# Optimization experiments

Measured on AMD Instinct MI355X. Metric: run time of the kernel, lower is better.

Reference implementation:

```python
import jax, jax.numpy as jnp
import numpy as np
from jax.scipy.special import logsumexp

# Model config: alphabet='ACGTZY', collapse='ACGTCA' -> 4 canonical bases, 2 mods
NBASE = 4
NTRANS = 2 * NBASE * (NBASE + 1)          # 40 flip-flop transition states
CAN_NMODS = np.array([1, 1, 0, 0])        # mods per canonical base (A:Y, C:Z)
SIZE = NTRANS + 1 + int(CAN_NMODS.sum())  # 43 linear outputs
LARGE_LOG_VAL = np.float32(50000.0)
T, N, INSIZE = 2000, 128, 256


def _can_indices():
    """Per-canonical-base index groups into the mod block of the linear output."""
    idx, cur = [], 0
    for nm in CAN_NMODS:
        idx.append(np.concatenate([[0], np.arange(cur + 1, cur + 1 + nm)]))
        cur += nm
    return idx

CAN_INDICES = _can_indices()


def setup_inputs() -> dict:
    key = jax.random.key(0)
    k1, k2, k3 = jax.random.split(key, 3)
    x = jax.random.normal(k1, (T, N, INSIZE), dtype=jnp.float32)
    W = jax.random.normal(k2, (SIZE, INSIZE), dtype=jnp.float32) / np.float32(INSIZE ** 0.5)
    b = jax.random.normal(k3, (SIZE,), dtype=jnp.float32) * 0.1
    return {"x": x, "W": W, "b": b}


def global_norm_flipflop(scores):
    """Log-partition of the flip-flop CRF via a sequential log-space scan.

    scores: (T, N, 2*nbase*(nbase+1)).
    """
    Tn, Nn, _ = scores.shape
    # initial state: flip states uniform, flop states ~ -inf
    fwd0 = jnp.concatenate(
        [jnp.zeros((Nn, NBASE), scores.dtype),
         jnp.full((Nn, NBASE), -LARGE_LOG_VAL, scores.dtype)], axis=1)
    logZ0 = logsumexp(fwd0, axis=1, keepdims=True)
    fwd0 = fwd0 - logZ0

    def step(carry, scores_t):
        fwd, logZ = carry
        # (N, nbase+1, 2*nbase): dest-state x source-state transition scores
        curr = fwd[:, None, :] + scores_t.reshape(Nn, NBASE + 1, 2 * NBASE)
        base1 = logsumexp(curr[:, :NBASE], axis=2)                    # to-flip states
        base2 = jnp.logaddexp(curr[:, NBASE, :NBASE],
                              curr[:, NBASE, NBASE:])                 # to-flop (stay)
        new = jnp.concatenate([base1, base2], axis=1)                 # (N, 2*nbase)
        fac = logsumexp(new, axis=1, keepdims=True)
        return (new - fac, logZ + fac), None

    (_, logZ), _ = jax.lax.scan(step, (fwd0, logZ0), scores)
    return scores - logZ / np.float32(Tn)


def reference(x, W, b):
    # Linear projection: (T, N, insize) -> (T, N, size)
    y = jnp.einsum('tnf,cf->tnc', x, W) + b
    # Globally-normalized flip-flop transition scores
    trans = global_norm_flipflop(y[:, :, :NTRANS])
    # Per-canonical-base categorical (can + its mods) log-softmax scores
    mods = [jax.nn.log_softmax(y[:, :, NTRANS + idx], axis=2) for idx in CAN_INDICES]
    return jnp.concatenate([trans] + mods, axis=2)
```

## Files before the change

kernel.cpp:

```cpp
#include <hip/hip_runtime.h>

#define T_DIM 2000
#define N_DIM 128
#define IN_DIM 256
#define OUT_C 46
#define NROWS (T_DIM * N_DIM)
#define NCHUNK 250
#define CLEN 8
#define NSUPER 25
#define SLEN 10

typedef short bf16x8 __attribute__((ext_vector_type(8)));
typedef float f32x4 __attribute__((ext_vector_type(4)));

union F8U { bf16x8 v; uint32_t u[4]; };

__device__ __forceinline__ uint32_t cvtpk(float lo, float hi) {
  uint32_t r;
  asm("v_cvt_pk_bf16_f32 %0, %1, %2" : "=v"(r) : "v"(lo), "v"(hi));
  return r;
}

__device__ __forceinline__ float bf2f(unsigned short u) {
  uint32_t w = (uint32_t)u << 16;
  return __builtin_bit_cast(float, w);
}

#define LDSK 264
#define YPAD 132

__global__ __launch_bounds__(256, 3) void k1_gemm(const float* __restrict__ x,
                                                  const float* __restrict__ W,
                                                  const float* __restrict__ b,
                                                  unsigned short* __restrict__ wsYT,
                                                  float* __restrict__ wsMod) {
  __shared__ unsigned short Wl[43 * LDSK];
  __shared__ unsigned short Yst[2 * 40 * YPAD];
  const int tid  = threadIdx.x;
  const int lane = tid & 63;
  const int wv   = tid >> 6;
  const int ln   = lane & 15;
  const int lh   = lane >> 4;

  {
    uint32_t* Wd = reinterpret_cast<uint32_t*>(Wl);
#pragma unroll
    for (int it = 0; it < 22; ++it) {
      int e = tid + it * 256;
      if (e < 43 * 128) {
        int n = e >> 7, kp = e & 127;
        float2 w = *reinterpret_cast<const float2*>(W + (size_t)n * IN_DIM + 2 * kp);
        Wd[n * (LDSK / 2) + kp] = cvtpk(w.x, w.y);
      }
    }
  }
  float bias[3];
#pragma unroll
  for (int nt = 0; nt < 3; ++nt) {
    int n = nt * 16 + ln;
    bias[nt] = b[n > 42 ? 42 : n];
  }
  __syncthreads();

  const int rowbase = blockIdx.x * 256 + wv * 64;
  const float* xbase = x + (size_t)(rowbase + ln) * IN_DIM + lh * 8;

  f32x4 bufA[8], bufB[8];
  f32x4 zero = {0.f, 0.f, 0.f, 0.f};
  f32x4 acc[3] = {zero, zero, zero};

#define LOADH(BUF, T, HF) do {                                               \
    const float* _p = xbase + (size_t)(T) * (16 * IN_DIM) + (HF) * 128;      \
    _Pragma("unroll")                                                        \
    for (int _s = 0; _s < 4; ++_s) {                                         \
      BUF[_s]     = *reinterpret_cast<const f32x4*>(_p + _s * 32);           \
      BUF[_s + 4] = *reinterpret_cast<const f32x4*>(_p + _s * 32 + 4);       \
    }                                                                        \
  } while (0)

#define COMPH(BUF, HF) do {                                                  \
    _Pragma("unroll")                                                        \
    for (int _s2 = 0; _s2 < 4; ++_s2) {                                      \
      F8U _af;                                                               \
      _af.u[0] = cvtpk(BUF[_s2].x, BUF[_s2].y);                              \
      _af.u[1] = cvtpk(BUF[_s2].z, BUF[_s2].w);                              \
      _af.u[2] = cvtpk(BUF[_s2 + 4].x, BUF[_s2 + 4].y);                      \
      _af.u[3] = cvtpk(BUF[_s2 + 4].z, BUF[_s2 + 4].w);                      \
      const int _s = (HF) * 4 + _s2;                                         \
      _Pragma("unroll")                                                      \
      for (int _nt = 0; _nt < 3; ++_nt) {                                    \
        const bf16x8 _bf = *reinterpret_cast<const bf16x8*>(                 \
            &Wl[(_nt * 16 + ln) * LDSK + _s * 32 + lh * 8]);                 \
        acc[_nt] = __builtin_amdgcn_mfma_f32_16x16x32_bf16(_af.v, _bf,       \
                                                           acc[_nt], 0, 0, 0);\
      }                                                                      \
    }                                                                        \
  } while (0)

  LOADH(bufA, 0, 0);
  LOADH(bufB, 0, 1);
#pragma unroll 1
  for (int t = 0; t < 4; ++t) {
    COMPH(bufA, 0);
    if (t < 3) LOADH(bufA, t + 1, 0);
    COMPH(bufB, 1);
    if (t < 3) LOADH(bufB, t + 1, 1);
    const int R0   = rowbase + t * 16;
    const int tloc = (R0 >> 7) & 1;
    const int n0   = (R0 & 127) + lh * 4;
#pragma unroll
    for (int nt = 0; nt < 3; ++nt) {
      const int c = nt * 16 + ln;
      if (nt < 2 || ln < 8) {
        uint32_t d0 = cvtpk(acc[nt][0] + bias[nt], acc[nt][1] + bias[nt]);
        uint32_t d1 = cvtpk(acc[nt][2] + bias[nt], acc[nt][3] + bias[nt]);
        uint2 v; v.x = d0; v.y = d1;
        *reinterpret_cast<uint2*>(&Yst[(tloc * 40 + c) * YPAD + n0]) = v;
      } else if (ln < 11) {
        const int tt = R0 >> 7;
        float4 v;
        v.x = acc[2][0] + bias[2]; v.y = acc[2][1] + bias[2];
        v.z = acc[2][2] + bias[2]; v.w = acc[2][3] + bias[2];
        *reinterpret_cast<float4*>(
            wsMod + ((size_t)tt * 3 + (ln - 8)) * 128 + n0) = v;
      }
      acc[nt] = zero;
    }
  }
#undef LOADH
#undef COMPH

  __syncthreads();
  uint2* gp = reinterpret_cast<uint2*>(wsYT + (size_t)blockIdx.x * (2 * 40 * 128));
  const uint2* lp = reinterpret_cast<const uint2*>(Yst);
#pragma unroll
  for (int it = 0; it < 10; ++it) {
    const int e   = tid + it * 256;
    const int row = e >> 5;
    const int q   = e & 31;
    gp[e] = lp[row * 33 + q];
  }
}

__global__ __launch_bounds__(128, 1) void k2a_chunk(const unsigned short* __restrict__ wsYT,
                                                    float* __restrict__ wsM,
                                                    float* __restrict__ wsScale) {
  const int c  = blockIdx.x;
  const int n  = threadIdx.x;
  const int t0 = c * CLEN;

  float M[8][8];
  float lsc = 0.f;
  float bufA[40], bufB[40];

#define LOADROW(BUF, TROW) do {                                              \
    const unsigned short* _yr = wsYT + (size_t)(TROW) * (40 * 128) + n;      \
    _Pragma("unroll")                                                        \
    for (int _q = 0; _q < 40; ++_q) BUF[_q] = bf2f(_yr[_q * 128]);           \
  } while (0)

#define INITM(BUF) do {                                                      \
    float _e[40];                                                            \
    _Pragma("unroll")                                                        \
    for (int _q = 0; _q < 40; ++_q) _e[_q] = __expf(BUF[_q]);                \
    _Pragma("unroll")                                                        \
    for (int _i = 0; _i < 4; ++_i)                                           \
      _Pragma("unroll")                                                      \
      for (int _j = 0; _j < 8; ++_j) M[_i][_j] = _e[8*_i+_j];                \
    _Pragma("unroll")                                                        \
    for (int _d = 0; _d < 4; ++_d) {                                         \
      _Pragma("unroll")                                                      \
      for (int _j = 0; _j < 8; ++_j) M[4+_d][_j] = 0.f;                      \
      M[4+_d][_d]   = _e[32+_d];                                             \
      M[4+_d][4+_d] = _e[36+_d];                                             \
    }                                                                        \
  } while (0)

#define STEPM(BUF) do {                                                      \
    float _e[40];                                                            \
    _Pragma("unroll")                                                        \
    for (int _q = 0; _q < 40; ++_q) _e[_q] = __expf(BUF[_q]);                \
    float _nm[8][8];                                                         \
    _Pragma("unroll")                                                        \
    for (int _j = 0; _j < 8; ++_j) {                                         \
      _Pragma("unroll")                                                      \
      for (int _i = 0; _i < 4; ++_i) {                                       \
        float _a = _e[8*_i+0]*M[0][_j] + _e[8*_i+1]*M[1][_j];                \
        float _b = _e[8*_i+2]*M[2][_j] + _e[8*_i+3]*M[3][_j];                \
        float _c = _e[8*_i+4]*M[4][_j] + _e[8*_i+5]*M[5][_j];                \
        float _d = _e[8*_i+6]*M[6][_j] + _e[8*_i+7]*M[7][_j];                \
        _nm[_i][_j] = (_a + _b) + (_c + _d);                                 \
      }                                                                      \
      _Pragma("unroll")                                                      \
      for (int _d2 = 0; _d2 < 4; ++_d2)                                      \
        _nm[4+_d2][_j] = _e[32+_d2]*M[_d2][_j] + _e[36+_d2]*M[4+_d2][_j];    \
    }                                                                        \
    _Pragma("unroll")                                                        \
    for (int _i = 0; _i < 8; ++_i)                                           \
      _Pragma("unroll")                                                      \
      for (int _j = 0; _j < 8; ++_j) M[_i][_j] = _nm[_i][_j];                \
  } while (0)

#define RENORM do {                                                          \
    float _S = 0.f;                                                          \
    _Pragma("unroll")                                                        \
    for (int _i = 0; _i < 8; ++_i)                                           \
      _Pragma("unroll")                                                      \
      for (int _j = 0; _j < 8; ++_j) _S += M[_i][_j];                        \
    lsc += __logf(_S);                                                       \
    const float _inv = 1.0f / _S;                                            \
    _Pragma("unroll")                                                        \
    for (int _i = 0; _i < 8; ++_i)                                           \
      _Pragma("unroll")                                                      \
      for (int _j = 0; _j < 8; ++_j) M[_i][_j] *= _inv;                      \
  } while (0)

  LOADROW(bufA, t0);
  LOADROW(bufB, t0 + 1);
  INITM(bufA);
  LOADROW(bufA, t0 + 2);
  STEPM(bufB);
  LOADROW(bufB, t0 + 3);
  STEPM(bufA);
  LOADROW(bufA, t0 + 4);
  STEPM(bufB);
  RENORM;
  LOADROW(bufB, t0 + 5);
  STEPM(bufA);
  LOADROW(bufA, t0 + 6);
  STEPM(bufB);
  LOADROW(bufB, t0 + 7);
  STEPM(bufA);
  STEPM(bufB);
  RENORM;

#undef LOADROW
#undef INITM
#undef STEPM
#undef RENORM

  float* dst = wsM + (size_t)(c * N_DIM + n) * 64;
#pragma unroll
  for (int q = 0; q < 16; ++q) {
    float4 v;
    v.x = M[q >> 1][(q & 1) * 4 + 0];
    v.y = M[q >> 1][(q & 1) * 4 + 1];
    v.z = M[q >> 1][(q & 1) * 4 + 2];
    v.w = M[q >> 1][(q & 1) * 4 + 3];
    reinterpret_cast<float4*>(dst)[q] = v;
  }
  wsScale[c * N_DIM + n] = lsc;
}

__global__ __launch_bounds__(128, 1) void k2c_super(const float* __restrict__ wsM,
                                                    const float* __restrict__ wsScale,
                                                    float* __restrict__ wsM2,
                                                    float* __restrict__ wsScale2) {
  const int sI = blockIdx.x;
  const int n  = threadIdx.x;
  const int c0 = sI * SLEN;

  float A[8][8], B0[8][8], B1[8][8];
  float lsc = 0.f;
#pragma unroll
  for (int u = 0; u < SLEN; ++u) lsc += wsScale[(c0 + u) * N_DIM + n];

#define LOADM(DST, CIDX) do {                                                \
    const float4* _p = reinterpret_cast<const float4*>(                      \
        wsM + (size_t)((CIDX) * N_DIM + n) * 64);                            \
    _Pragma("unroll")                                                        \
    for (int _q = 0; _q < 16; ++_q) {                                        \
      float4 _v = _p[_q];                                                    \
      DST[_q >> 1][(_q & 1) * 4 + 0] = _v.x;                                 \
      DST[_q >> 1][(_q & 1) * 4 + 1] = _v.y;                                 \
      DST[_q >> 1][(_q & 1) * 4 + 2] = _v.z;                                 \
      DST[_q >> 1][(_q & 1) * 4 + 3] = _v.w;                                 \
    }                                                                        \
  } while (0)

#define FOLD(BB) do {                                                        \
    float C[8][8];                                                           \
    _Pragma("unroll")                                                        \
    for (int _i = 0; _i < 8; ++_i)                                           \
      _Pragma("unroll")                                                      \
      for (int _j = 0; _j < 8; ++_j) {                                       \
        float _a = BB[_i][0]*A[0][_j] + BB[_i][1]*A[1][_j];                  \
        float _b = BB[_i][2]*A[2][_j] + BB[_i][3]*A[3][_j];                  \
        float _c = BB[_i][4]*A[4][_j] + BB[_i][5]*A[5][_j];                  \
        float _d = BB[_i][6]*A[6][_j] + BB[_i][7]*A[7][_j];                  \
        C[_i][_j] = (_a + _b) + (_c + _d);                                   \
      }                                                                      \
    float _S = 0.f;                                                          \
    _Pragma("unroll")                                                        \
    for (int _i = 0; _i < 8; ++_i)                                           \
      _Pragma("unroll")                                                      \
      for (int _j = 0; _j < 8; ++_j) _S += C[_i][_j];                        \
    lsc += __logf(_S);                                                       \
    const float _inv = 1.0f / _S;                                            \
    _Pragma("unroll")                                                        \
    for (int _i = 0; _i < 8; ++_i)                                           \
      _Pragma("unroll")                                                      \
      for (int _j = 0; _j < 8; ++_j) A[_i][_j] = C[_i][_j] * _inv;           \
  } while (0)

  LOADM(A, c0);
  LOADM(B0, c0 + 1);
  LOADM(B1, c0 + 2);
  FOLD(B0); LOADM(B0, c0 + 3);
  FOLD(B1); LOADM(B1, c0 + 4);
  FOLD(B0); LOADM(B0, c0 + 5);
  FOLD(B1); LOADM(B1, c0 + 6);
  FOLD(B0); LOADM(B0, c0 + 7);
  FOLD(B1); LOADM(B1, c0 + 8);
  FOLD(B0); LOADM(B0, c0 + 9);
  FOLD(B1);
  FOLD(B0);
#undef LOADM
#undef FOLD

  float* dst = wsM2 + (size_t)(sI * N_DIM + n) * 64;
#pragma unroll
  for (int q = 0; q < 16; ++q) {
    float4 v;
    v.x = A[q >> 1][(q & 1) * 4 + 0];
    v.y = A[q >> 1][(q & 1) * 4 + 1];
    v.z = A[q >> 1][(q & 1) * 4 + 2];
    v.w = A[q >> 1][(q & 1) * 4 + 3];
    reinterpret_cast<float4*>(dst)[q] = v;
  }
  wsScale2[sI * N_DIM + n] = lsc;
}

__global__ __launch_bounds__(128, 1) void k2b_fold(const float* __restrict__ wsM2,
                                                   const float* __restrict__ wsScale2,
                                                   float* __restrict__ wsLZ) {
  const int tid = threadIdx.x;
  const int n = blockIdx.x * 16 + (tid >> 3);
  const int i = tid & 7;
  const int gbase = (tid & 63) & ~7;

  float4 r0[NSUPER], r1[NSUPER];
  float sc[NSUPER];
#pragma unroll
  for (int s = 0; s < NSUPER; ++s) {
    const float* Mp = wsM2 + ((size_t)(s * N_DIM + n) * 64 + i * 8);
    r0[s] = *reinterpret_cast<const float4*>(Mp);
    r1[s] = *reinterpret_cast<const float4*>(Mp + 4);
    sc[s] = wsScale2[s * N_DIM + n];
  }

  float p[8] = {1.f, 1.f, 1.f, 1.f, 0.f, 0.f, 0.f, 0.f};
  float lz = 0.f;
#pragma unroll
  for (int s = 0; s < NSUPER; ++s) {
    float np = r0[s].x * p[0] + r0[s].y * p[1] + r0[s].z * p[2] + r0[s].w * p[3]
             + r1[s].x * p[4] + r1[s].y * p[5] + r1[s].z * p[6] + r1[s].w * p[7];
#pragma unroll
    for (int j = 0; j < 8; ++j) p[j] = __shfl(np, gbase + j, 64);
    float S = ((p[0] + p[1]) + (p[2] + p[3])) + ((p[4] + p[5]) + (p[6] + p[7]));
    lz += __logf(S) + sc[s];
    const float inv = 1.0f / S;
#pragma unroll
    for (int j = 0; j < 8; ++j) p[j] *= inv;
  }
  if (i == 0) wsLZ[n] = lz * (1.0f / (float)T_DIM);
}

__global__ __launch_bounds__(256, 3) void k3_out(const unsigned short* __restrict__ wsYT,
                                                 const float* __restrict__ wsMod,
                                                 const float* __restrict__ wsLZ,
                                                 float* __restrict__ out) {
  __shared__ float L[256 * 47];
  const int tid = threadIdx.x;
  const int fr  = blockIdx.x * 256 + tid;
  const int t   = fr >> 7;
  const int n   = fr & 127;
  const float sub = wsLZ[n];

  const unsigned short* yr = wsYT + (size_t)t * (40 * 128) + n;
  float* lrow = &L[tid * 47];
#pragma unroll
  for (int c = 0; c < 40; ++c) lrow[c] = bf2f(yr[c * 128]) - sub;

  const float* mp = wsMod + (size_t)t * (3 * 128) + n;
  const float y40 = mp[0], y41 = mp[128], y42 = mp[256];
  const float m01 = fmaxf(y40, y41);
  const float l01 = m01 + log1pf(__expf(fminf(y40, y41) - m01));
  const float m02 = fmaxf(y40, y42);
  const float l02 = m02 + log1pf(__expf(fminf(y40, y42) - m02));
  lrow[40] = y40 - l01;
  lrow[41] = y41 - l01;
  lrow[42] = y40 - l02;
  lrow[43] = y42 - l02;
  lrow[44] = 0.f;
  lrow[45] = 0.f;
  __syncthreads();

  const size_t base = (size_t)blockIdx.x * (256 * 46);
#pragma unroll
  for (int j = 0; j < 46; ++j) {
    const int e = j * 256 + tid;
    const int r = e / 46;
    const int c = e - r * 46;
    __builtin_nontemporal_store(L[r * 47 + c], &out[base + e]);
  }
}

extern "C" void kernel_launch(void* const* d_in, const int* in_sizes, int n_in,
                              void* d_out, int out_size, void* d_ws, size_t ws_size,
                              hipStream_t stream) {
  (void)in_sizes; (void)n_in; (void)out_size; (void)ws_size;
  const float* x = (const float*)d_in[0];
  const float* W = (const float*)d_in[1];
  const float* b = (const float*)d_in[2];
  float* out = (float*)d_out;

  char* wsb = (char*)d_ws;
  unsigned short* wsYT = (unsigned short*)wsb;
  float* wsMod   = (float*)(wsb + (size_t)T_DIM * 40 * 128 * 2);
  float* wsM     = wsMod + (size_t)T_DIM * 3 * N_DIM;
  float* wsScale = wsM + (size_t)NCHUNK * N_DIM * 64;
  float* wsM2    = wsScale + NCHUNK * N_DIM;
  float* wsScale2= wsM2 + (size_t)NSUPER * N_DIM * 64;
  float* wsLZ    = wsScale2 + NSUPER * N_DIM;

  hipLaunchKernelGGL(k1_gemm,   dim3(NROWS / 256), dim3(256), 0, stream,
                     x, W, b, wsYT, wsMod);
  hipLaunchKernelGGL(k2a_chunk, dim3(NCHUNK), dim3(128), 0, stream,
                     wsYT, wsM, wsScale);
  hipLaunchKernelGGL(k2c_super, dim3(NSUPER), dim3(128), 0, stream,
                     wsM, wsScale, wsM2, wsScale2);
  hipLaunchKernelGGL(k2b_fold,  dim3(8), dim3(128), 0, stream,
                     wsM2, wsScale2, wsLZ);
  hipLaunchKernelGGL(k3_out,    dim3(NROWS / 256), dim3(256), 0, stream,
                     wsYT, wsMod, wsLZ, out);
}
```

Measured before the change: 100.0 us.

## Halve GEMM LDS staging buffer, flush per timestep, raise occupancy to four blocks

The GEMM kernel now stages only one timestep (40x128 bf16) in shared memory instead of two. Each wave now covers 32 rows across both timesteps, and the main loop is fully unrolled with an intermediate flush to global memory plus extra barriers. The smaller LDS footprint lets launch bounds request four blocks per CU instead of three, aiming to hide memory latency better. In exchange it adds two barriers and tighter register limits, which may cause spills.

```diff
diff --git a/kernel.cpp b/kernel.cpp
--- a/kernel.cpp
+++ b/kernel.cpp
@@ -29,13 +29,13 @@
 #define LDSK 264
 #define YPAD 132
 
-__global__ __launch_bounds__(256, 3) void k1_gemm(const float* __restrict__ x,
+__global__ __launch_bounds__(256, 4) void k1_gemm(const float* __restrict__ x,
                                                   const float* __restrict__ W,
                                                   const float* __restrict__ b,
                                                   unsigned short* __restrict__ wsYT,
                                                   float* __restrict__ wsMod) {
   __shared__ unsigned short Wl[43 * LDSK];
-  __shared__ unsigned short Yst[2 * 40 * YPAD];
+  __shared__ unsigned short Yst[40 * YPAD];
   const int tid  = threadIdx.x;
   const int lane = tid & 63;
   const int wv   = tid >> 6;
@@ -62,15 +62,16 @@
   }
   __syncthreads();
 
-  const int rowbase = blockIdx.x * 256 + wv * 64;
-  const float* xbase = x + (size_t)(rowbase + ln) * IN_DIM + lh * 8;
+  const int base = blockIdx.x * 256;
+  const float* xbase = x + (size_t)(base + wv * 32 + ln) * IN_DIM + lh * 8;
 
   f32x4 bufA[8], bufB[8];
   f32x4 zero = {0.f, 0.f, 0.f, 0.f};
   f32x4 acc[3] = {zero, zero, zero};
 
-#define LOADH(BUF, T, HF) do {                                               \
-    const float* _p = xbase + (size_t)(T) * (16 * IN_DIM) + (HF) * 128;      \
+#define LOADH(BUF, K, HF) do {                                               \
+    const float* _p = xbase +                                                \
+        (size_t)(((K) >> 1) * 128 + ((K) & 1) * 16) * IN_DIM + (HF) * 128;   \
     _Pragma("unroll")                                                        \
     for (int _s = 0; _s < 4; ++_s) {                                         \
       BUF[_s]     = *reinterpret_cast<const f32x4*>(_p + _s * 32);           \
@@ -97,49 +98,64 @@
     }                                                                        \
   } while (0)
 
+#define EPILOG(K) do {                                                       \
+    const int _n0 = wv * 32 + ((K) & 1) * 16 + lh * 4;                       \
+    _Pragma("unroll")                                                        \
+    for (int _nt = 0; _nt < 3; ++_nt) {                                      \
+      if (_nt < 2 || ln < 8) {                                               \
+        const int _c = _nt * 16 + ln;                                        \
+        uint32_t _d0 = cvtpk(acc[_nt][0] + bias[_nt], acc[_nt][1] + bias[_nt]);\
+        uint32_t _d1 = cvtpk(acc[_nt][2] + bias[_nt], acc[_nt][3] + bias[_nt]);\
+        uint2 _v; _v.x = _d0; _v.y = _d1;                                    \
+        *reinterpret_cast<uint2*>(&Yst[_c * YPAD + _n0]) = _v;               \
+      } else if (ln < 11) {                                                  \
+        const int _tt = blockIdx.x * 2 + ((K) >> 1);                         \
+        float4 _v;                                                           \
+        _v.x = acc[2][0] + bias[2]; _v.y = acc[2][1] + bias[2];              \
+        _v.z = acc[2][2] + bias[2]; _v.w = acc[2][3] + bias[2];              \
+        *reinterpret_cast<float4*>(                                          \
+            wsMod + ((size_t)_tt * 3 + (ln - 8)) * 128 + _n0) = _v;          \
+      }                                                                      \
+      acc[_nt] = zero;                                                       \
+    }                                                                        \
+  } while (0)
+
+#define FLUSH(TT) do {                                                       \
+    uint2* _gp = reinterpret_cast<uint2*>(wsYT + (size_t)(TT) * (40 * 128)); \
+    const uint2* _lp = reinterpret_cast<const uint2*>(Yst);                  \
+    _Pragma("unroll")                                                        \
+    for (int _it = 0; _it < 5; ++_it) {                                      \
+      const int _e   = tid + _it * 256;                                      \
+      const int _row = _e >> 5;                                              \
+      const int _q   = _e & 31;                                              \
+      _gp[_e] = _lp[_row * 33 + _q];                                         \
+    }                                                                        \
+  } while (0)
+
   LOADH(bufA, 0, 0);
   LOADH(bufB, 0, 1);
-#pragma unroll 1
-  for (int t = 0; t < 4; ++t) {
-    COMPH(bufA, 0);
-    if (t < 3) LOADH(bufA, t + 1, 0);
-    COMPH(bufB, 1);
-    if (t < 3) LOADH(bufB, t + 1, 1);
-    const int R0   = rowbase + t * 16;
-    const int tloc = (R0 >> 7) & 1;
-    const int n0   = (R0 & 127) + lh * 4;
-#pragma unroll
-    for (int nt = 0; nt < 3; ++nt) {
-      const int c = nt * 16 + ln;
-      if (nt < 2 || ln < 8) {
-        uint32_t d0 = cvtpk(acc[nt][0] + bias[nt], acc[nt][1] + bias[nt]);
-        uint32_t d1 = cvtpk(acc[nt][2] + bias[nt], acc[nt][3] + bias[nt]);
-        uint2 v; v.x = d0; v.y = d1;
-        *reinterpret_cast<uint2*>(&Yst[(tloc * 40 + c) * YPAD + n0]) = v;
-      } else if (ln < 11) {
-        const int tt = R0 >> 7;
-        float4 v;
-        v.x = acc[2][0] + bias[2]; v.y = acc[2][1] + bias[2];
-        v.z = acc[2][2] + bias[2]; v.w = acc[2][3] + bias[2];
-        *reinterpret_cast<float4*>(
-            wsMod + ((size_t)tt * 3 + (ln - 8)) * 128 + n0) = v;
-      }
-      acc[nt] = zero;
-    }
-  }
+  COMPH(bufA, 0); LOADH(bufA, 1, 0);
+  COMPH(bufB, 1); LOADH(bufB, 1, 1);
+  EPILOG(0);
+  COMPH(bufA, 0); LOADH(bufA, 2, 0);
+  COMPH(bufB, 1); LOADH(bufB, 2, 1);
+  EPILOG(1);
+  __syncthreads();
+  FLUSH(blockIdx.x * 2 + 0);
+  __syncthreads();
+  COMPH(bufA, 0); LOADH(bufA, 3, 0);
+  COMPH(bufB, 1); LOADH(bufB, 3, 1);
+  EPILOG(2);
+  COMPH(bufA, 0);
+  COMPH(bufB, 1);
+  EPILOG(3);
+  __syncthreads();
+  FLUSH(blockIdx.x * 2 + 1);
+
 #undef LOADH
 #undef COMPH
-
-  __syncthreads();
-  uint2* gp = reinterpret_cast<uint2*>(wsYT + (size_t)blockIdx.x * (2 * 40 * 128));
-  const uint2* lp = reinterpret_cast<const uint2*>(Yst);
-#pragma unroll
-  for (int it = 0; it < 10; ++it) {
-    const int e   = tid + it * 256;
-    const int row = e >> 5;
-    const int q   = e & 31;
-    gp[e] = lp[row * 33 + q];
-  }
+#undef EPILOG
+#undef FLUSH
 }
 
 __global__ __launch_bounds__(128, 1) void k2a_chunk(const unsigned short* __restrict__ wsYT,
```

After: 100.7 us. No clear change (+0.7%).
